# Performance work log

Hardware: AMD Instinct MI355X
Metric: run time of the kernel (lower is better)

## Reference

```python
import jax, jax.numpy as jnp
import numpy as np

# dims: M=512 new tokens, N=2048 model dim, D=128 head dim, H=16 heads,
# L=4096 cache length, P=2048 cache write offset

def setup_inputs() -> dict:
    key = jax.random.key(0)
    k0, k1, k2, k3 = jax.random.split(key, 4)
    M, N, D, L = 512, 2048, 128, 4096
    X = jax.random.normal(k0, (M, N), jnp.float32)
    # scale weights ~1/sqrt(N) so projections have unit-ish scale
    W_qkv = jax.random.normal(k1, (N, 3 * N), jnp.float32) * (N ** -0.5)
    H = N // D
    cache_K = jax.random.normal(k2, (H, L, D), jnp.float32)
    # realistic cache state: keys stored in cache are RMS-normalized
    cache_K = cache_K * jax.lax.rsqrt(jnp.mean(cache_K * cache_K, axis=-1, keepdims=True))
    cache_V = jax.random.normal(k3, (H, L, D), jnp.float32)
    return {"X": X, "W_qkv": W_qkv, "cache_K": cache_K, "cache_V": cache_V, "P": 2048}


def reference(X, W_qkv, cache_K, cache_V, P):
    M = X.shape[0]
    H, L, D = cache_K.shape
    qkv = X @ W_qkv                              # [M, 3N]
    q, k, v = jnp.split(qkv, 3, axis=-1)         # each [M, N]
    q = q.reshape(M, H, D).transpose(1, 0, 2)    # [H, M, D]
    k = k.reshape(M, H, D).transpose(1, 0, 2)
    v = v.reshape(M, H, D).transpose(1, 0, 2)
    # RMS-style normalization (no learned gain, no eps in original)
    q = q * jax.lax.rsqrt(jnp.mean(q * q, axis=-1, keepdims=True))
    k = k * jax.lax.rsqrt(jnp.mean(k * k, axis=-1, keepdims=True))
    # scatter-update into KV cache at position P
    Kc = jax.lax.dynamic_update_slice(cache_K, k, (0, P, 0))  # [H, L, D]
    Vc = jax.lax.dynamic_update_slice(cache_V, v, (0, P, 0))
    # unmasked, unscaled attention over the full cache (faithful to original:
    # plain exp/sum, no max-subtraction, no 1/sqrt(D))
    scores = jnp.einsum('hmd,hld->hml', q, Kc)   # [H, M, L]
    w = jnp.exp(scores)
    w = w / jnp.sum(w, axis=-1, keepdims=True)
    out = jnp.einsum('hml,hld->hmd', w, Vc)      # [H, M, D]
    return out.transpose(1, 0, 2).reshape(M, H * D)
```

## Files before the change

kernel.cpp:

```cpp
#include <hip/hip_runtime.h>
#include <math.h>

typedef _Float16 half_t;
typedef _Float16 half8 __attribute__((ext_vector_type(8)));
typedef _Float16 half4_t __attribute__((ext_vector_type(4)));
typedef _Float16 half2_t __attribute__((ext_vector_type(2)));
typedef float floatx4 __attribute__((ext_vector_type(4)));

#define M_TOK 512
#define N_DIM 2048
#define D_HEAD 128
#define H_HEADS 16
#define L_CACHE 4096
#define THREE_N 6144
#define NCHUNK 16
#define LCHUNK 256

__global__ __launch_bounds__(256) void prep_kernel(const float* __restrict__ cK,
                                                   const float* __restrict__ cV,
                                                   const float* __restrict__ W,
                                                   const float* __restrict__ X,
                                                   half_t* __restrict__ K16,
                                                   half_t* __restrict__ V16T,
                                                   half_t* __restrict__ W16T,
                                                   half_t* __restrict__ X16) {
    __shared__ half_t tile[32 * 36];
    int b = blockIdx.x;
    int t = threadIdx.x;

    if (b < 8192) {
        size_t i = ((size_t)b * 256 + t) * 4;
        float4 v = *(const float4*)(cK + i);
        half4_t h = {(half_t)v.x, (half_t)v.y, (half_t)v.z, (half_t)v.w};
        *(half4_t*)(K16 + i) = h;
        return;
    }
    b -= 8192;
    if (b < 1024) {
        size_t i = ((size_t)b * 256 + t) * 4;
        float4 v = *(const float4*)(X + i);
        half4_t h = {(half_t)v.x, (half_t)v.y, (half_t)v.z, (half_t)v.w};
        *(half4_t*)(X16 + i) = h;
        return;
    }
    b -= 1024;
    if (b < 8192) {
        int h = b >> 9;
        int rem = b & 511;
        int lt = rem >> 2, dt = rem & 3;
        int l0 = lt * 32, d0 = dt * 32;
        {
            int li = t >> 3, c4 = (t & 7) * 4;
            float4 v = *(const float4*)(cV + ((size_t)h * L_CACHE + l0 + li) * D_HEAD + d0 + c4);
            tile[li * 36 + c4 + 0] = (half_t)v.x;
            tile[li * 36 + c4 + 1] = (half_t)v.y;
            tile[li * 36 + c4 + 2] = (half_t)v.z;
            tile[li * 36 + c4 + 3] = (half_t)v.w;
        }
        __syncthreads();
        {
            int di = t >> 3, lj = (t & 7) * 4;
            half4_t o = {tile[(lj + 0) * 36 + di], tile[(lj + 1) * 36 + di],
                         tile[(lj + 2) * 36 + di], tile[(lj + 3) * 36 + di]};
            *(half4_t*)(V16T + ((size_t)h * D_HEAD + d0 + di) * L_CACHE + l0 + lj) = o;
        }
        return;
    }
    b -= 8192;
    {
        int n0 = (b % 192) * 32, k0 = (b / 192) * 32;
        {
            int ki = t >> 3, n4 = (t & 7) * 4;
            float4 v = *(const float4*)(W + (size_t)(k0 + ki) * THREE_N + n0 + n4);
            tile[ki * 36 + n4 + 0] = (half_t)v.x;
            tile[ki * 36 + n4 + 1] = (half_t)v.y;
            tile[ki * 36 + n4 + 2] = (half_t)v.z;
            tile[ki * 36 + n4 + 3] = (half_t)v.w;
        }
        __syncthreads();
        {
            int ni = t >> 3, k4 = (t & 7) * 4;
            half4_t o = {tile[(k4 + 0) * 36 + ni], tile[(k4 + 1) * 36 + ni],
                         tile[(k4 + 2) * 36 + ni], tile[(k4 + 3) * 36 + ni]};
            *(half4_t*)(W16T + (size_t)(n0 + ni) * N_DIM + k0 + k4) = o;
        }
    }
}

__global__ __launch_bounds__(256) void gemm_fused_kernel(const half_t* __restrict__ X16,
                                                         const half_t* __restrict__ W16T,
                                                         const int* __restrict__ Pp,
                                                         half_t* __restrict__ Q16,
                                                         half_t* __restrict__ K16,
                                                         half_t* __restrict__ V16T) {
    __shared__ half_t As[64 * 72];
    __shared__ half_t Bs[128 * 72];
    __shared__ half_t Vt[128 * 72];
    __shared__ float ssbuf[4][32];
    const int t = threadIdx.x;
    const int wid = t >> 6, lane = t & 63;
    const int quad = lane >> 4, ln = lane & 15;
    const int bx = blockIdx.x, by = blockIdx.y;
    const int m0 = by * 64, n0 = bx * 128;
    const int wm = (wid >> 1) * 32, wn = (wid & 1) * 64;

    floatx4 acc[2][4] = {};

    const int ar = t >> 3, ag = (t & 7) * 8;
    const int br = t >> 3, bg = (t & 7) * 8;

    for (int k0 = 0; k0 < N_DIM; k0 += 64) {
        __syncthreads();
#pragma unroll
        for (int p = 0; p < 2; ++p) {
            int r = ar + p * 32;
            *(half8*)&As[r * 72 + ag] =
                *(const half8*)(X16 + (size_t)(m0 + r) * N_DIM + k0 + ag);
        }
#pragma unroll
        for (int p = 0; p < 4; ++p) {
            int r = br + p * 32;
            *(half8*)&Bs[r * 72 + bg] =
                *(const half8*)(W16T + (size_t)(n0 + r) * N_DIM + k0 + bg);
        }
        __syncthreads();
#pragma unroll
        for (int kt = 0; kt < 2; ++kt) {
            half8 a[2], b[4];
#pragma unroll
            for (int i = 0; i < 2; ++i)
                a[i] = *(half8*)&As[(wm + i * 16 + ln) * 72 + kt * 32 + quad * 8];
#pragma unroll
            for (int j = 0; j < 4; ++j)
                b[j] = *(half8*)&Bs[(wn + j * 16 + ln) * 72 + kt * 32 + quad * 8];
#pragma unroll
            for (int i = 0; i < 2; ++i)
#pragma unroll
                for (int j = 0; j < 4; ++j)
                    acc[i][j] = __builtin_amdgcn_mfma_f32_16x16x32_f16(a[i], b[j], acc[i][j], 0, 0, 0);
        }
    }

    const int seg = bx >> 4, h = bx & 15;
    const int P = *Pp;

    if (seg < 2) {
        float ss[2][4], scale[2][4];
#pragma unroll
        for (int i = 0; i < 2; ++i)
#pragma unroll
            for (int r = 0; r < 4; ++r) {
                float s = 0.f;
#pragma unroll
                for (int j = 0; j < 4; ++j) s += acc[i][j][r] * acc[i][j][r];
#pragma unroll
                for (int msk = 1; msk < 16; msk <<= 1) s += __shfl_xor(s, msk, 64);
                ss[i][r] = s;
            }
        if (ln == 0) {
#pragma unroll
            for (int i = 0; i < 2; ++i)
#pragma unroll
                for (int r = 0; r < 4; ++r)
                    ssbuf[wid][i * 16 + quad * 4 + r] = ss[i][r];
        }
        __syncthreads();
#pragma unroll
        for (int i = 0; i < 2; ++i)
#pragma unroll
            for (int r = 0; r < 4; ++r)
                scale[i][r] =
                    rsqrtf((ss[i][r] + ssbuf[wid ^ 1][i * 16 + quad * 4 + r]) * (1.0f / 128.0f));
#pragma unroll
        for (int i = 0; i < 2; ++i) {
            int mbase = m0 + wm + i * 16 + quad * 4;
#pragma unroll
            for (int j = 0; j < 4; ++j) {
                int col = wn + j * 16 + ln;
#pragma unroll
                for (int r = 0; r < 4; ++r) {
                    int m = mbase + r;
                    half_t val = (half_t)(acc[i][j][r] * scale[i][r]);
                    if (seg == 0)
                        Q16[((size_t)h * M_TOK + m) * D_HEAD + col] = val;
                    else
                        K16[((size_t)h * L_CACHE + P + m) * D_HEAD + col] = val;
                }
            }
        }
    } else {
#pragma unroll
        for (int i = 0; i < 2; ++i) {
            int mbase = wm + i * 16 + quad * 4;
#pragma unroll
            for (int j = 0; j < 4; ++j) {
                int d = wn + j * 16 + ln;
#pragma unroll
                for (int r = 0; r < 4; ++r)
                    Vt[d * 72 + mbase + r] = (half_t)acc[i][j][r];
            }
        }
        __syncthreads();
#pragma unroll
        for (int p = 0; p < 4; ++p) {
            int s = p * 256 + t;
            int d = s >> 3, sg = s & 7;
            *(half8*)(V16T + ((size_t)h * D_HEAD + d) * L_CACHE + P + m0 + sg * 8) =
                *(half8*)&Vt[d * 72 + sg * 8];
        }
    }
}

__global__ __launch_bounds__(256) void attn_partial_kernel(const half_t* __restrict__ Q16,
                                                           const half_t* __restrict__ K16,
                                                           const half_t* __restrict__ V16T,
                                                           half_t* __restrict__ Opart,
                                                           float* __restrict__ mstat,
                                                           float* __restrict__ lstat) {
    __shared__ half_t Ks[64 * 136];
    __shared__ half_t Vs[128 * 72];
    __shared__ half_t Ps[4 * 16 * 72];
    const int t = threadIdx.x, w = t >> 6, lane = t & 63;
    const int quad = lane >> 4, ln = lane & 15;
    const int h = blockIdx.y, c = blockIdx.z;
    const int mb = blockIdx.x * 128;
    const half_t* Qh = Q16 + (size_t)h * M_TOK * D_HEAD;
    const half_t* Kh = K16 + (size_t)h * L_CACHE * D_HEAD;
    const half_t* Vh = V16T + (size_t)h * D_HEAD * L_CACHE;

    half8 qf[2][4];
#pragma unroll
    for (int s = 0; s < 2; ++s) {
        int m0 = mb + s * 64 + w * 16;
#pragma unroll
        for (int dt = 0; dt < 4; ++dt)
            qf[s][dt] = *(const half8*)(Qh + (size_t)(m0 + ln) * D_HEAD + dt * 32 + quad * 8);
    }

    floatx4 oacc[2][8] = {};
    float mrow[2][4], lrow[2][4];
#pragma unroll
    for (int s = 0; s < 2; ++s)
#pragma unroll
        for (int r = 0; r < 4; ++r) { mrow[s][r] = -INFINITY; lrow[s][r] = 0.f; }

    half_t* Pw = Ps + w * (16 * 72);

    for (int l0 = c * LCHUNK; l0 < (c + 1) * LCHUNK; l0 += 64) {
        __syncthreads();
        {
            int lr = t >> 4, ch = t & 15;
#pragma unroll
            for (int p = 0; p < 4; ++p, lr += 16)
                *(half8*)&Ks[lr * 136 + ch * 8] =
                    *(const half8*)(Kh + (size_t)(l0 + lr) * D_HEAD + ch * 8);
        }
        {
            int dr = t >> 3, ch = t & 7;
#pragma unroll
            for (int p = 0; p < 4; ++p, dr += 32)
                *(half8*)&Vs[dr * 72 + ch * 8] =
                    *(const half8*)(Vh + (size_t)dr * L_CACHE + l0 + ch * 8);
        }
        __syncthreads();

#pragma unroll
        for (int s = 0; s < 2; ++s) {
            floatx4 sacc[4] = {};
#pragma unroll
            for (int nt = 0; nt < 4; ++nt)
#pragma unroll
                for (int dt = 0; dt < 4; ++dt) {
                    half8 b = *(half8*)&Ks[(nt * 16 + ln) * 136 + dt * 32 + quad * 8];
                    sacc[nt] = __builtin_amdgcn_mfma_f32_16x16x32_f16(qf[s][dt], b, sacc[nt], 0, 0, 0);
                }

            float alpha[4];
#pragma unroll
            for (int r = 0; r < 4; ++r) {
                float mx = fmaxf(fmaxf(sacc[0][r], sacc[1][r]), fmaxf(sacc[2][r], sacc[3][r]));
#pragma unroll
                for (int msk = 8; msk; msk >>= 1) mx = fmaxf(mx, __shfl_xor(mx, msk, 16));
                float mnew = fmaxf(mrow[s][r], mx);
                alpha[r] = __expf(mrow[s][r] - mnew);
                mrow[s][r] = mnew;
                float psum = 0.f;
#pragma unroll
                for (int nt = 0; nt < 4; ++nt) {
                    float p = __expf(sacc[nt][r] - mnew);
                    sacc[nt][r] = p;
                    psum += p;
                }
#pragma unroll
                for (int msk = 8; msk; msk >>= 1) psum += __shfl_xor(psum, msk, 16);
                lrow[s][r] = lrow[s][r] * alpha[r] + psum;
            }

#pragma unroll
            for (int nt = 0; nt < 4; ++nt)
#pragma unroll
                for (int r = 0; r < 4; ++r)
                    Pw[(quad * 4 + r) * 72 + nt * 16 + ln] = (half_t)sacc[nt][r];

#pragma unroll
            for (int nt8 = 0; nt8 < 8; ++nt8)
#pragma unroll
                for (int r = 0; r < 4; ++r)
                    oacc[s][nt8][r] *= alpha[r];

#pragma unroll
            for (int kt = 0; kt < 2; ++kt) {
                half8 a = *(half8*)&Pw[ln * 72 + kt * 32 + quad * 8];
#pragma unroll
                for (int nt8 = 0; nt8 < 8; ++nt8) {
                    half8 b = *(half8*)&Vs[(nt8 * 16 + ln) * 72 + kt * 32 + quad * 8];
                    oacc[s][nt8] = __builtin_amdgcn_mfma_f32_16x16x32_f16(a, b, oacc[s][nt8], 0, 0, 0);
                }
            }
        }
    }

    half_t* Oc = Opart + ((size_t)(c * H_HEADS + h) * M_TOK) * D_HEAD;
    float* ms = mstat + (size_t)(c * H_HEADS + h) * M_TOK;
    float* ls = lstat + (size_t)(c * H_HEADS + h) * M_TOK;
#pragma unroll
    for (int s = 0; s < 2; ++s) {
        int m0 = mb + s * 64 + w * 16;
#pragma unroll
        for (int nt8 = 0; nt8 < 8; ++nt8) {
            int col = nt8 * 16 + ln;
#pragma unroll
            for (int r = 0; r < 4; ++r)
                Oc[(size_t)(m0 + quad * 4 + r) * D_HEAD + col] = (half_t)oacc[s][nt8][r];
        }
        if (ln == 0) {
#pragma unroll
            for (int r = 0; r < 4; ++r) {
                ms[m0 + quad * 4 + r] = mrow[s][r];
                ls[m0 + quad * 4 + r] = lrow[s][r];
            }
        }
    }
}

__global__ __launch_bounds__(256) void combine_kernel(const half_t* __restrict__ Opart,
                                                      const float* __restrict__ mstat,
                                                      const float* __restrict__ lstat,
                                                      float* __restrict__ out) {
    int gw = blockIdx.x * 4 + (threadIdx.x >> 6);
    int lane = threadIdx.x & 63;
    int h = gw >> 9, m = gw & 511;
    int d = lane * 2;

    float ms[NCHUNK];
    float mg = -INFINITY;
#pragma unroll
    for (int c = 0; c < NCHUNK; ++c) {
        ms[c] = mstat[((c * H_HEADS + h) << 9) + m];
        mg = fmaxf(mg, ms[c]);
    }
    float denom = 0.f, o0 = 0.f, o1 = 0.f;
#pragma unroll
    for (int c = 0; c < NCHUNK; ++c) {
        float e = __expf(ms[c] - mg);
        denom += lstat[((c * H_HEADS + h) << 9) + m] * e;
        const half_t* Oc = Opart + (((size_t)(c * H_HEADS + h) << 9) + m) * D_HEAD + d;
        half2_t v = *(const half2_t*)Oc;
        o0 += (float)v.x * e;
        o1 += (float)v.y * e;
    }
    float inv = 1.0f / denom;
    float* op = out + (size_t)m * N_DIM + h * D_HEAD + d;
    op[0] = o0 * inv;
    op[1] = o1 * inv;
}

extern "C" void kernel_launch(void* const* d_in, const int* in_sizes, int n_in,
                              void* d_out, int out_size, void* d_ws, size_t ws_size,
                              hipStream_t stream) {
    const float* X = (const float*)d_in[0];
    const float* W = (const float*)d_in[1];
    const float* cK = (const float*)d_in[2];
    const float* cV = (const float*)d_in[3];
    const int* Pp = (const int*)d_in[4];
    float* out = (float*)d_out;

    char* ws = (char*)d_ws;
    half_t* Q16 = (half_t*)(ws + 0);
    half_t* K16 = (half_t*)(ws + 2097152);
    half_t* V16T = (half_t*)(ws + 18874368);
    half_t* X16 = (half_t*)(ws + 35651584);
    half_t* W16T = (half_t*)(ws + 37748736);
    half_t* Opart = (half_t*)(ws + 37748736);
    float* mstat = (float*)(ws + 71303168);
    float* lstat = (float*)(ws + 71827456);

    prep_kernel<<<29696, 256, 0, stream>>>(cK, cV, W, X, K16, V16T, W16T, X16);
    gemm_fused_kernel<<<dim3(48, 8), 256, 0, stream>>>(X16, W16T, Pp, Q16, K16, V16T);
    attn_partial_kernel<<<dim3(4, 16, NCHUNK), 256, 0, stream>>>(Q16, K16, V16T, Opart, mstat, lstat);
    combine_kernel<<<2048, 256, 0, stream>>>(Opart, mstat, lstat, out);
}
```

Measured before the change: 242.0 us.

## Reorder attention grid, make partial-result layout chunk-contiguous, and alias GEMM LDS buffers

The attention partial kernel now puts the cache chunk index on the fastest grid dimension, so blocks launched together cover different K/V chunks of the same head. Partial outputs and m/l statistics are stored with the chunk index innermost per (head, token). This lets the combine kernel read each row's partials contiguously instead of striding across chunk-sized planes. The GEMM kernel also reuses the A-tile LDS region for the V transpose buffer, with an added barrier, to shrink shared memory and possibly raise occupancy. The cost is more scattered stores in the partial kernel, since each 256-byte row segment lands in a different place.

```diff
diff --git a/kernel.cpp b/kernel.cpp
--- a/kernel.cpp
+++ b/kernel.cpp
@@ -93,10 +93,11 @@
                                                          half_t* __restrict__ Q16,
                                                          half_t* __restrict__ K16,
                                                          half_t* __restrict__ V16T) {
-    __shared__ half_t As[64 * 72];
-    __shared__ half_t Bs[128 * 72];
-    __shared__ half_t Vt[128 * 72];
+    __shared__ half_t smem[64 * 72 + 128 * 72];
     __shared__ float ssbuf[4][32];
+    half_t* As = smem;
+    half_t* Bs = smem + 64 * 72;
+    half_t* Vt = smem;
     const int t = threadIdx.x;
     const int wid = t >> 6, lane = t & 63;
     const int quad = lane >> 4, ln = lane & 15;
@@ -189,6 +190,7 @@
             }
         }
     } else {
+        __syncthreads();
 #pragma unroll
         for (int i = 0; i < 2; ++i) {
             int mbase = wm + i * 16 + quad * 4;
@@ -222,8 +224,8 @@
     __shared__ half_t Ps[4 * 16 * 72];
     const int t = threadIdx.x, w = t >> 6, lane = t & 63;
     const int quad = lane >> 4, ln = lane & 15;
-    const int h = blockIdx.y, c = blockIdx.z;
-    const int mb = blockIdx.x * 128;
+    const int c = blockIdx.x, h = blockIdx.y;
+    const int mb = blockIdx.z * 128;
     const half_t* Qh = Q16 + (size_t)h * M_TOK * D_HEAD;
     const half_t* Kh = K16 + (size_t)h * L_CACHE * D_HEAD;
     const half_t* Vh = V16T + (size_t)h * D_HEAD * L_CACHE;
@@ -320,9 +322,6 @@
         }
     }
 
-    half_t* Oc = Opart + ((size_t)(c * H_HEADS + h) * M_TOK) * D_HEAD;
-    float* ms = mstat + (size_t)(c * H_HEADS + h) * M_TOK;
-    float* ls = lstat + (size_t)(c * H_HEADS + h) * M_TOK;
 #pragma unroll
     for (int s = 0; s < 2; ++s) {
         int m0 = mb + s * 64 + w * 16;
@@ -330,14 +329,18 @@
         for (int nt8 = 0; nt8 < 8; ++nt8) {
             int col = nt8 * 16 + ln;
 #pragma unroll
-            for (int r = 0; r < 4; ++r)
-                Oc[(size_t)(m0 + quad * 4 + r) * D_HEAD + col] = (half_t)oacc[s][nt8][r];
+            for (int r = 0; r < 4; ++r) {
+                int m = m0 + quad * 4 + r;
+                Opart[(((size_t)h * M_TOK + m) * NCHUNK + c) * D_HEAD + col] =
+                    (half_t)oacc[s][nt8][r];
+            }
         }
         if (ln == 0) {
 #pragma unroll
             for (int r = 0; r < 4; ++r) {
-                ms[m0 + quad * 4 + r] = mrow[s][r];
-                ls[m0 + quad * 4 + r] = lrow[s][r];
+                int m = m0 + quad * 4 + r;
+                mstat[((size_t)h * M_TOK + m) * NCHUNK + c] = mrow[s][r];
+                lstat[((size_t)h * M_TOK + m) * NCHUNK + c] = lrow[s][r];
             }
         }
     }
@@ -352,20 +355,23 @@
     int h = gw >> 9, m = gw & 511;
     int d = lane * 2;
 
+    const float* msp = mstat + (size_t)gw * NCHUNK;
+    const float* lsp = lstat + (size_t)gw * NCHUNK;
+    const half_t* Ob = Opart + (size_t)gw * NCHUNK * D_HEAD;
+
     float ms[NCHUNK];
     float mg = -INFINITY;
 #pragma unroll
     for (int c = 0; c < NCHUNK; ++c) {
-        ms[c] = mstat[((c * H_HEADS + h) << 9) + m];
+        ms[c] = msp[c];
         mg = fmaxf(mg, ms[c]);
     }
     float denom = 0.f, o0 = 0.f, o1 = 0.f;
 #pragma unroll
     for (int c = 0; c < NCHUNK; ++c) {
         float e = __expf(ms[c] - mg);
-        denom += lstat[((c * H_HEADS + h) << 9) + m] * e;
-        const half_t* Oc = Opart + (((size_t)(c * H_HEADS + h) << 9) + m) * D_HEAD + d;
-        half2_t v = *(const half2_t*)Oc;
+        denom += lsp[c] * e;
+        half2_t v = *(const half2_t*)(Ob + c * D_HEAD + d);
         o0 += (float)v.x * e;
         o1 += (float)v.y * e;
     }
@@ -397,6 +403,6 @@
 
     prep_kernel<<<29696, 256, 0, stream>>>(cK, cV, W, X, K16, V16T, W16T, X16);
     gemm_fused_kernel<<<dim3(48, 8), 256, 0, stream>>>(X16, W16T, Pp, Q16, K16, V16T);
-    attn_partial_kernel<<<dim3(4, 16, NCHUNK), 256, 0, stream>>>(Q16, K16, V16T, Opart, mstat, lstat);
+    attn_partial_kernel<<<dim3(16, 16, 4), 256, 0, stream>>>(Q16, K16, V16T, Opart, mstat, lstat);
     combine_kernel<<<2048, 256, 0, stream>>>(Opart, mstat, lstat, out);
 }
```

After: 249.4 us. 3.0% more time.

## Read fp32 K cache directly in attention and drop separate K conversion pass

Applied to the files above, without the earlier changes.

Removes the prep stage that converted the whole K cache to fp16. The GEMM now writes the normalized new K rows in fp32 straight into the input cache buffer, and attention converts K tiles to fp16 while loading them into shared memory. The prep transposes for V and W use larger 128-row tiles with wider stores, the GEMM shares one shared-memory region between As and Vt, and the attention grid is flattened with a head/chunk-interleaved mapping. This cuts one full read-write pass over K, but attention global reads of K double and the input buffer is mutated in place.

```diff
diff --git a/kernel.cpp b/kernel.cpp
--- a/kernel.cpp
+++ b/kernel.cpp
@@ -16,26 +16,16 @@
 #define NCHUNK 16
 #define LCHUNK 256
 
-__global__ __launch_bounds__(256) void prep_kernel(const float* __restrict__ cK,
-                                                   const float* __restrict__ cV,
+__global__ __launch_bounds__(256) void prep_kernel(const float* __restrict__ cV,
                                                    const float* __restrict__ W,
                                                    const float* __restrict__ X,
-                                                   half_t* __restrict__ K16,
                                                    half_t* __restrict__ V16T,
                                                    half_t* __restrict__ W16T,
                                                    half_t* __restrict__ X16) {
-    __shared__ half_t tile[32 * 36];
+    __shared__ half_t tile[128 * 36];
     int b = blockIdx.x;
     int t = threadIdx.x;
 
-    if (b < 8192) {
-        size_t i = ((size_t)b * 256 + t) * 4;
-        float4 v = *(const float4*)(cK + i);
-        half4_t h = {(half_t)v.x, (half_t)v.y, (half_t)v.z, (half_t)v.w};
-        *(half4_t*)(K16 + i) = h;
-        return;
-    }
-    b -= 8192;
     if (b < 1024) {
         size_t i = ((size_t)b * 256 + t) * 4;
         float4 v = *(const float4*)(X + i);
@@ -44,45 +34,59 @@
         return;
     }
     b -= 1024;
-    if (b < 8192) {
-        int h = b >> 9;
-        int rem = b & 511;
-        int lt = rem >> 2, dt = rem & 3;
-        int l0 = lt * 32, d0 = dt * 32;
-        {
-            int li = t >> 3, c4 = (t & 7) * 4;
-            float4 v = *(const float4*)(cV + ((size_t)h * L_CACHE + l0 + li) * D_HEAD + d0 + c4);
-            tile[li * 36 + c4 + 0] = (half_t)v.x;
-            tile[li * 36 + c4 + 1] = (half_t)v.y;
-            tile[li * 36 + c4 + 2] = (half_t)v.z;
-            tile[li * 36 + c4 + 3] = (half_t)v.w;
-        }
-        __syncthreads();
-        {
-            int di = t >> 3, lj = (t & 7) * 4;
-            half4_t o = {tile[(lj + 0) * 36 + di], tile[(lj + 1) * 36 + di],
-                         tile[(lj + 2) * 36 + di], tile[(lj + 3) * 36 + di]};
-            *(half4_t*)(V16T + ((size_t)h * D_HEAD + d0 + di) * L_CACHE + l0 + lj) = o;
+    if (b < 2048) {
+        int h = b >> 7;
+        int rem = b & 127;
+        int l0 = (rem >> 2) * 128, d0 = (rem & 3) * 32;
+        {
+            int row = t >> 1, q = (t & 1) * 16;
+            const float* src = cV + ((size_t)h * L_CACHE + l0 + row) * D_HEAD + d0 + q;
+#pragma unroll
+            for (int i = 0; i < 4; ++i) {
+                float4 v = *(const float4*)(src + 4 * i);
+                half4_t hv = {(half_t)v.x, (half_t)v.y, (half_t)v.z, (half_t)v.w};
+                *(half4_t*)&tile[row * 36 + q + 4 * i] = hv;
+            }
+        }
+        __syncthreads();
+        {
+            int drow = t >> 3, seg = (t & 7) * 16;
+#pragma unroll
+            for (int j = 0; j < 2; ++j) {
+                half8 o;
+#pragma unroll
+                for (int kk = 0; kk < 8; ++kk)
+                    o[kk] = tile[(seg + j * 8 + kk) * 36 + drow];
+                *(half8*)(V16T + ((size_t)h * D_HEAD + d0 + drow) * L_CACHE + l0 + seg + j * 8) = o;
+            }
         }
         return;
     }
-    b -= 8192;
+    b -= 2048;
     {
-        int n0 = (b % 192) * 32, k0 = (b / 192) * 32;
-        {
-            int ki = t >> 3, n4 = (t & 7) * 4;
-            float4 v = *(const float4*)(W + (size_t)(k0 + ki) * THREE_N + n0 + n4);
-            tile[ki * 36 + n4 + 0] = (half_t)v.x;
-            tile[ki * 36 + n4 + 1] = (half_t)v.y;
-            tile[ki * 36 + n4 + 2] = (half_t)v.z;
-            tile[ki * 36 + n4 + 3] = (half_t)v.w;
-        }
-        __syncthreads();
-        {
-            int ni = t >> 3, k4 = (t & 7) * 4;
-            half4_t o = {tile[(k4 + 0) * 36 + ni], tile[(k4 + 1) * 36 + ni],
-                         tile[(k4 + 2) * 36 + ni], tile[(k4 + 3) * 36 + ni]};
-            *(half4_t*)(W16T + (size_t)(n0 + ni) * N_DIM + k0 + k4) = o;
+        int kt = b / 192, nt = b % 192;
+        int k0 = kt * 128, n0 = nt * 32;
+        {
+            int row = t >> 1, q = (t & 1) * 16;
+            const float* src = W + (size_t)(k0 + row) * THREE_N + n0 + q;
+#pragma unroll
+            for (int i = 0; i < 4; ++i) {
+                float4 v = *(const float4*)(src + 4 * i);
+                half4_t hv = {(half_t)v.x, (half_t)v.y, (half_t)v.z, (half_t)v.w};
+                *(half4_t*)&tile[row * 36 + q + 4 * i] = hv;
+            }
+        }
+        __syncthreads();
+        {
+            int nrow = t >> 3, seg = (t & 7) * 16;
+#pragma unroll
+            for (int j = 0; j < 2; ++j) {
+                half8 o;
+#pragma unroll
+                for (int kk = 0; kk < 8; ++kk)
+                    o[kk] = tile[(seg + j * 8 + kk) * 36 + nrow];
+                *(half8*)(W16T + (size_t)(n0 + nrow) * N_DIM + k0 + seg + j * 8) = o;
+            }
         }
     }
 }
@@ -91,12 +95,13 @@
                                                          const half_t* __restrict__ W16T,
                                                          const int* __restrict__ Pp,
                                                          half_t* __restrict__ Q16,
-                                                         half_t* __restrict__ K16,
+                                                         float* __restrict__ cacheK,
                                                          half_t* __restrict__ V16T) {
-    __shared__ half_t As[64 * 72];
-    __shared__ half_t Bs[128 * 72];
-    __shared__ half_t Vt[128 * 72];
+    __shared__ half_t smem[64 * 72 + 128 * 72];
     __shared__ float ssbuf[4][32];
+    half_t* As = smem;
+    half_t* Bs = smem + 64 * 72;
+    half_t* Vt = smem;
     const int t = threadIdx.x;
     const int wid = t >> 6, lane = t & 63;
     const int quad = lane >> 4, ln = lane & 15;
@@ -180,15 +185,16 @@
 #pragma unroll
                 for (int r = 0; r < 4; ++r) {
                     int m = mbase + r;
-                    half_t val = (half_t)(acc[i][j][r] * scale[i][r]);
+                    float v = acc[i][j][r] * scale[i][r];
                     if (seg == 0)
-                        Q16[((size_t)h * M_TOK + m) * D_HEAD + col] = val;
+                        Q16[((size_t)h * M_TOK + m) * D_HEAD + col] = (half_t)v;
                     else
-                        K16[((size_t)h * L_CACHE + P + m) * D_HEAD + col] = val;
+                        cacheK[((size_t)h * L_CACHE + P + m) * D_HEAD + col] = v;
                 }
             }
         }
     } else {
+        __syncthreads();
 #pragma unroll
         for (int i = 0; i < 2; ++i) {
             int mbase = wm + i * 16 + quad * 4;
@@ -212,7 +218,7 @@
 }
 
 __global__ __launch_bounds__(256) void attn_partial_kernel(const half_t* __restrict__ Q16,
-                                                           const half_t* __restrict__ K16,
+                                                           const float* __restrict__ cacheK,
                                                            const half_t* __restrict__ V16T,
                                                            half_t* __restrict__ Opart,
                                                            float* __restrict__ mstat,
@@ -222,10 +228,12 @@
     __shared__ half_t Ps[4 * 16 * 72];
     const int t = threadIdx.x, w = t >> 6, lane = t & 63;
     const int quad = lane >> 4, ln = lane & 15;
-    const int h = blockIdx.y, c = blockIdx.z;
-    const int mb = blockIdx.x * 128;
+    const int f = blockIdx.x;
+    const int pair = (f >> 5) * 8 + (f & 7);
+    const int c = pair >> 4, h = pair & 15;
+    const int mb = ((f >> 3) & 3) * 128;
     const half_t* Qh = Q16 + (size_t)h * M_TOK * D_HEAD;
-    const half_t* Kh = K16 + (size_t)h * L_CACHE * D_HEAD;
+    const float* Kh = cacheK + (size_t)h * L_CACHE * D_HEAD;
     const half_t* Vh = V16T + (size_t)h * D_HEAD * L_CACHE;
 
     half8 qf[2][4];
@@ -249,11 +257,16 @@
     for (int l0 = c * LCHUNK; l0 < (c + 1) * LCHUNK; l0 += 64) {
         __syncthreads();
         {
-            int lr = t >> 4, ch = t & 15;
-#pragma unroll
-            for (int p = 0; p < 4; ++p, lr += 16)
-                *(half8*)&Ks[lr * 136 + ch * 8] =
-                    *(const half8*)(Kh + (size_t)(l0 + lr) * D_HEAD + ch * 8);
+            int lr = t >> 4, ch = (t & 15) * 8;
+#pragma unroll
+            for (int p = 0; p < 4; ++p, lr += 16) {
+                const float* src = Kh + (size_t)(l0 + lr) * D_HEAD + ch;
+                float4 a = *(const float4*)src;
+                float4 bq = *(const float4*)(src + 4);
+                half8 hv = {(half_t)a.x, (half_t)a.y, (half_t)a.z, (half_t)a.w,
+                            (half_t)bq.x, (half_t)bq.y, (half_t)bq.z, (half_t)bq.w};
+                *(half8*)&Ks[lr * 136 + ch] = hv;
+            }
         }
         {
             int dr = t >> 3, ch = t & 7;
@@ -380,23 +393,22 @@
                               hipStream_t stream) {
     const float* X = (const float*)d_in[0];
     const float* W = (const float*)d_in[1];
-    const float* cK = (const float*)d_in[2];
+    float* cK = (float*)d_in[2];
     const float* cV = (const float*)d_in[3];
     const int* Pp = (const int*)d_in[4];
     float* out = (float*)d_out;
 
     char* ws = (char*)d_ws;
     half_t* Q16 = (half_t*)(ws + 0);
-    half_t* K16 = (half_t*)(ws + 2097152);
-    half_t* V16T = (half_t*)(ws + 18874368);
-    half_t* X16 = (half_t*)(ws + 35651584);
-    half_t* W16T = (half_t*)(ws + 37748736);
-    half_t* Opart = (half_t*)(ws + 37748736);
-    float* mstat = (float*)(ws + 71303168);
-    float* lstat = (float*)(ws + 71827456);
-
-    prep_kernel<<<29696, 256, 0, stream>>>(cK, cV, W, X, K16, V16T, W16T, X16);
-    gemm_fused_kernel<<<dim3(48, 8), 256, 0, stream>>>(X16, W16T, Pp, Q16, K16, V16T);
-    attn_partial_kernel<<<dim3(4, 16, NCHUNK), 256, 0, stream>>>(Q16, K16, V16T, Opart, mstat, lstat);
+    half_t* V16T = (half_t*)(ws + 2097152);
+    half_t* X16 = (half_t*)(ws + 18874368);
+    half_t* W16T = (half_t*)(ws + 20971520);
+    half_t* Opart = (half_t*)(ws + 20971520);
+    float* mstat = (float*)(ws + 54525952);
+    float* lstat = (float*)(ws + 55050240);
+
+    prep_kernel<<<6144, 256, 0, stream>>>(cV, W, X, V16T, W16T, X16);
+    gemm_fused_kernel<<<dim3(48, 8), 256, 0, stream>>>(X16, W16T, Pp, Q16, cK, V16T);
+    attn_partial_kernel<<<1024, 256, 0, stream>>>(Q16, cK, V16T, Opart, mstat, lstat);
     combine_kernel<<<2048, 256, 0, stream>>>(Opart, mstat, lstat, out);
 }
```

Result: slower. 261.5 us (+8.0%).
